# Kernel optimization log

Measured on AMD Instinct MI355X. Metric: run time of the kernel, lower is better.

Reference implementation:

```python
import jax, jax.numpy as jnp
import numpy as np

B, S, N, C, D = 1, 6, 10000, 128, 4
HEADS, PTS = 4, 8
HF, WF = 28, 50
M = HF * WF


def setup_inputs() -> dict:
    key0 = jax.random.key(0)
    ks = jax.random.split(key0, 14)
    sc = C ** -0.5
    d = {}
    d["query"] = jax.random.normal(ks[0], (B, N, C), jnp.float32)
    d["key"] = jax.random.normal(ks[1], (S, M, B, C), jnp.float32)
    d["value"] = jax.random.normal(ks[2], (S, M, B, C), jnp.float32)
    d["query_pos"] = jax.random.normal(ks[3], (B, N, C), jnp.float32) * 0.1
    d["reference_points_cam"] = jax.random.uniform(ks[4], (S, B, N, D, 2), jnp.float32, -0.2, 1.2)
    d["bev_mask"] = jax.random.randint(ks[5], (S, B, N, D), 0, 2).astype(bool)
    d["w_off"] = jax.random.normal(ks[6], (C, HEADS * PTS * 2), jnp.float32) * sc
    d["b_off"] = jax.random.normal(ks[7], (HEADS * PTS * 2,), jnp.float32) * 0.01
    d["w_attn"] = jax.random.normal(ks[8], (C, HEADS * PTS), jnp.float32) * sc
    d["b_attn"] = jax.random.normal(ks[9], (HEADS * PTS,), jnp.float32) * 0.01
    d["w_val"] = jax.random.normal(ks[10], (C, C), jnp.float32) * sc
    d["b_val"] = jax.random.normal(ks[11], (C,), jnp.float32) * 0.01
    d["w_out"] = jax.random.normal(ks[12], (C, C), jnp.float32) * sc
    d["b_out"] = jax.random.normal(ks[13], (C,), jnp.float32) * 0.01
    d["Hf"] = HF
    d["Wf"] = WF
    return d


def reference(query, key, value, query_pos, reference_points_cam, bev_mask,
              w_off, b_off, w_attn, b_attn, w_val, b_val, w_out, b_out, Hf, Wf):
    # SpatialCrossAttention with MSDeformAttn3D (BEVFormer semantics, eval mode: dropout=identity).
    # The torch data-dependent gather/rebatch/scatter is replaced by mathematically equivalent
    # masked computation: deformable attention is per-query independent, so running it for all
    # BEV queries per camera and mask-accumulating yields identical slots.
    B_, N_, C_ = query.shape
    S_ = key.shape[0]
    D_ = reference_points_cam.shape[3]
    H, P = HEADS, PTS
    dh = C_ // H
    Pd = P // D_
    q = query + query_pos  # (B,N,C)
    off = (q @ w_off + b_off).reshape(B_, N_, H, Pd, D_, 2)
    aw = jax.nn.softmax((q @ w_attn + b_attn).reshape(B_, N_, H, P), axis=-1)  # over levels*points (L=1)
    # value projection; per-camera feature maps laid out as (B,S,H,Hf*Wf,dh)
    v = jnp.transpose(value, (2, 0, 1, 3))  # (B,S,M,C)
    v = v @ w_val + b_val
    v = v.reshape(B_, S_, Hf * Wf, H, dh).transpose(0, 1, 3, 2, 4)  # (B,S,H,M,dh)
    ref = jnp.transpose(reference_points_cam, (1, 0, 2, 3, 4))  # (B,S,N,D,2)
    norm = jnp.array([Wf, Hf], jnp.float32)  # offset_normalizer = (W, H)
    loc = ref[:, :, :, None, None, :, :] + off[:, None] / norm  # (B,S,N,H,Pd,D,2)
    loc = loc.reshape(B_, S_, N_, H, P, 2)
    # bilinear sampling, zero padding, align_corners=False
    ix = loc[..., 0] * Wf - 0.5
    iy = loc[..., 1] * Hf - 0.5
    x0 = jnp.floor(ix)
    y0 = jnp.floor(iy)

    def flat(a):  # (B,S,N,H,P) -> (B,S,H,N*P)
        return a.transpose(0, 1, 3, 2, 4).reshape(B_, S_, H, N_ * P)

    def gather(xi, yi):
        ok = (xi >= 0) & (xi < Wf) & (yi >= 0) & (yi < Hf)
        xi_c = jnp.clip(xi, 0, Wf - 1).astype(jnp.int32)
        yi_c = jnp.clip(yi, 0, Hf - 1).astype(jnp.int32)
        idx = flat(yi_c * Wf + xi_c)
        g = jnp.take_along_axis(v, idx[..., None], axis=3)  # (B,S,H,N*P,dh)
        return g * flat(ok.astype(v.dtype))[..., None]

    wx1 = ix - x0
    wy1 = iy - y0
    wx0 = 1.0 - wx1
    wy0 = 1.0 - wy1
    samp = (gather(x0, y0) * flat(wx0 * wy0)[..., None]
            + gather(x0 + 1, y0) * flat(wx1 * wy0)[..., None]
            + gather(x0, y0 + 1) * flat(wx0 * wy1)[..., None]
            + gather(x0 + 1, y0 + 1) * flat(wx1 * wy1)[..., None])  # (B,S,H,N*P,dh)
    samp = samp.reshape(B_, S_, H, N_, P, dh)
    out = jnp.einsum('bshnpd,bnhp->bsnhd', samp, aw).reshape(B_, S_, N_, C_)
    # masked scatter-accumulate back to BEV slots
    mask = jnp.transpose(jnp.any(bev_mask, axis=-1), (1, 0, 2))  # (B,S,N)
    slots = jnp.sum(out * mask[..., None].astype(out.dtype), axis=1)  # (B,N,C)
    count = jnp.maximum(mask.astype(out.dtype).sum(axis=1), 1.0)
    slots = slots / count[..., None]
    return slots @ w_out + b_out + query  # dropout is identity in eval
```

## Files before the change

kernel.cpp:

```cpp
#include <hip/hip_runtime.h>
#include <math.h>

#define S_ 6
#define N_ 10000
#define C_ 128
#define D_ 4
#define H_ 4
#define P_ 8
#define HF_ 28
#define WF_ 50
#define M_ (HF_ * WF_)
#define DH_ 32
#define SM_ (S_ * M_)
#define QB_ 8
#define ABYTES (S_ * H_ * M_ * 32)

#define NB_V ((SM_ + 31) / 32)
#define NB_O ((N_ + 31) / 32)

typedef float floatx2 __attribute__((ext_vector_type(2)));
typedef _Float16 half4v __attribute__((ext_vector_type(4)));

template <int NC, int MT, int MR, int MODE>
__device__ __forceinline__ void gemm_body(
    const float* __restrict__ A, const float* __restrict__ A2,
    const float* __restrict__ B0, const float* __restrict__ B1,
    const float* __restrict__ bias0, const float* __restrict__ bias1,
    float* __restrict__ outf, char* __restrict__ out8,
    int Mrows, int m0, int tid, int nthreads, float (*Alds)[132]) {
  constexpr int NTHR = (NC / 4) * (MT / MR);

  for (int i = tid; i < MT * 32; i += nthreads) {
    int r = i >> 5, k = (i & 31) * 4;
    int row = m0 + r;
    float4 v = make_float4(0.f, 0.f, 0.f, 0.f);
    if (row < Mrows) {
      v = *(const float4*)(A + (size_t)row * C_ + k);
      if (MODE == 1) {
        float4 v2 = *(const float4*)(A2 + (size_t)row * C_ + k);
        v.x += v2.x; v.y += v2.y; v.z += v2.z; v.w += v2.w;
      }
    }
    *(float4*)(&Alds[r][k]) = v;
  }
  __syncthreads();
  if (tid >= NTHR) return;

  int ci = tid % (NC / 4);
  int mi = tid / (NC / 4);
  int c0 = ci * 4, r0 = mi * MR;

  const float* bs;
  if (MODE == 1) bs = (c0 < 64) ? bias0 + c0 : bias1 + (c0 - 64);
  else bs = bias0 + c0;

  float acc[MR][4];
#pragma unroll
  for (int j = 0; j < MR; ++j)
#pragma unroll
    for (int cc = 0; cc < 4; ++cc) acc[j][cc] = bs[cc];

#pragma unroll 2
  for (int k4 = 0; k4 < C_; k4 += 4) {
    float bf[16];
#pragma unroll
    for (int kk = 0; kk < 4; ++kk) {
      int k = k4 + kk;
      float4 b4;
      if (MODE == 1)
        b4 = (c0 < 64) ? *(const float4*)(B0 + (size_t)k * 64 + c0)
                       : *(const float4*)(B1 + (size_t)k * 32 + (c0 - 64));
      else
        b4 = *(const float4*)(B0 + (size_t)k * NC + c0);
      bf[kk * 4 + 0] = b4.x; bf[kk * 4 + 1] = b4.y;
      bf[kk * 4 + 2] = b4.z; bf[kk * 4 + 3] = b4.w;
    }
    float af[MR * 4];
#pragma unroll
    for (int j = 0; j < MR; ++j) {
      float4 a4 = *(const float4*)(&Alds[r0 + j][k4]);
      af[j * 4 + 0] = a4.x; af[j * 4 + 1] = a4.y;
      af[j * 4 + 2] = a4.z; af[j * 4 + 3] = a4.w;
    }
#pragma unroll
    for (int j = 0; j < MR; ++j)
#pragma unroll
      for (int kk = 0; kk < 4; ++kk)
#pragma unroll
        for (int cc = 0; cc < 4; ++cc)
          acc[j][cc] = fmaf(af[j * 4 + kk], bf[kk * 4 + cc], acc[j][cc]);
  }

#pragma unroll
  for (int j = 0; j < MR; ++j) {
    int row = m0 + r0 + j;
    if (row >= Mrows) continue;
    if (MODE == 0) {
      int s = row / M_, mm = row % M_;
      int y = mm / WF_, x = mm % WF_;
      int h = c0 >> 5, d0 = c0 & 31;
      int w = __builtin_amdgcn_cvt_pk_fp8_f32(acc[j][0], acc[j][1], 0, false);
      w = __builtin_amdgcn_cvt_pk_fp8_f32(acc[j][2], acc[j][3], w, true);
      size_t hm = (size_t)s * H_ + h;
      *(int*)(out8 + (hm * M_ + mm) * 32 + d0) = w;
      if (x > 0) {
        int kp = (x - 1) >> 1, slot = 1 - (x & 1);
        *(int*)(out8 + ABYTES + ((hm * HF_ + y) * 25 + kp) * 64 +
                slot * 32 + d0) = w;
      }
    } else if (MODE == 1) {
      *(float4*)(outf + (size_t)row * 96 + c0) =
          make_float4(acc[j][0], acc[j][1], acc[j][2], acc[j][3]);
    }
  }
}

__global__ __launch_bounds__(256) void prep_kernel(
    const float* __restrict__ value, const float* __restrict__ w_val,
    const float* __restrict__ b_val, char* __restrict__ vh8,
    const float* __restrict__ query, const float* __restrict__ query_pos,
    const float* __restrict__ w_off, const float* __restrict__ b_off,
    const float* __restrict__ w_attn, const float* __restrict__ b_attn,
    float* __restrict__ OFFL) {
  __shared__ float Alds[32][132];
  int bid = blockIdx.x;
  if (bid < NB_V) {
    gemm_body<128, 32, 4, 0>(value, nullptr, w_val, nullptr, b_val, nullptr,
                             nullptr, vh8, SM_, bid * 32, threadIdx.x, 256,
                             Alds);
  } else {
    gemm_body<96, 32, 4, 1>(query, query_pos, w_off, w_attn, b_off, b_attn,
                            OFFL, nullptr, N_, (bid - NB_V) * 32, threadIdx.x,
                            256, Alds);
  }
}

__global__ __launch_bounds__(256) void attn2_kernel(
    const float* __restrict__ OFFL,
    const float* __restrict__ refpts,
    const int*   __restrict__ bev_mask,
    const char*  __restrict__ vh8,
    const float* __restrict__ query,
    const float* __restrict__ w_out,
    const float* __restrict__ b_out,
    float* __restrict__ out) {
  int n0 = blockIdx.x * QB_;
  int tid = threadIdx.x;

  __shared__ float off[QB_][64];
  __shared__ float logits[QB_][32];
  __shared__ float aw[QB_][32];
  __shared__ float refl[QB_][48];
  __shared__ int smask[QB_][6];
  __shared__ int2 sidx[QB_][194];
  __shared__ half4v swh[QB_][194];
  __shared__ float sl[QB_][132];

  for (int i = tid; i < QB_ * 96; i += 256) {
    int q = i / 96, c = i % 96;
    float v = OFFL[(size_t)(n0 + q) * 96 + c];
    if (c < 64) off[q][c] = v; else logits[q][c - 64] = v;
  }
  for (int i = tid; i < QB_ * 48; i += 256) {
    int q = i / 48, rem = i % 48;
    int s = rem >> 3, r8 = rem & 7;
    refl[q][rem] = refpts[((size_t)s * N_ + (n0 + q)) * 8 + r8];
  }
  if (tid < QB_ * 6) {
    int q = tid / 6, s = tid % 6;
    const int* bm = bev_mask + ((size_t)s * N_ + (n0 + q)) * D_;
    smask[q][s] = (bm[0] | bm[1] | bm[2] | bm[3]) ? 1 : 0;
  }
  __syncthreads();

  {
    int q = tid >> 5, j = tid & 31, h = j >> 3;
    float mx = -1e30f;
#pragma unroll
    for (int p = 0; p < P_; ++p) mx = fmaxf(mx, logits[q][h * P_ + p]);
    float sum = 0.f;
#pragma unroll
    for (int p = 0; p < P_; ++p) sum += expf(logits[q][h * P_ + p] - mx);
    aw[q][j] = expf(logits[q][j] - mx) / sum;
  }
  __syncthreads();

  for (int i = tid; i < QB_ * 192; i += 256) {
    int q = i / 192, j = i % 192;
    int s = j >> 5, w32 = j & 31, p = w32 >> 2, h = w32 & 3;
    int pd = p >> 2, dd = p & 3;
    float rx = refl[q][s * 8 + dd * 2 + 0];
    float ry = refl[q][s * 8 + dd * 2 + 1];
    float ox = off[q][h * 16 + pd * 8 + dd * 2 + 0];
    float oy = off[q][h * 16 + pd * 8 + dd * 2 + 1];
    float ix = rx * (float)WF_ + ox - 0.5f;
    float iy = ry * (float)HF_ + oy - 0.5f;
    float x0f = floorf(ix), y0f = floorf(iy);
    int x0 = (int)x0f, y0 = (int)y0f;
    float wx1 = ix - x0f, wy1 = iy - y0f;
    float wx0 = 1.f - wx1, wy0 = 1.f - wy1;
    float a = aw[q][h * P_ + p];
    bool vx0 = (x0 >= 0) && (x0 < WF_);
    bool vx1 = (x0 + 1 >= 0) && (x0 + 1 < WF_);
    bool vy0 = (y0 >= 0) && (y0 < HF_);
    bool vy1 = (y0 + 1 >= 0) && (y0 + 1 < HF_);
    int y0c = min(max(y0, 0), HF_ - 1);
    int y1c = min(max(y0 + 1, 0), HF_ - 1);
    int hm = s * H_ + h;
    int itop, ibot;
    if (x0 >= 0 && x0 <= WF_ - 2 && !(x0 & 1)) {
      itop = (hm * M_ + y0c * WF_ + x0) * 32;
      ibot = (hm * M_ + y1c * WF_ + x0) * 32;
    } else if (x0 >= 1 && x0 <= WF_ - 1 && (x0 & 1)) {
      int kp = (x0 - 1) >> 1;
      itop = ABYTES + ((hm * HF_ + y0c) * 25 + kp) * 64;
      ibot = ABYTES + ((hm * HF_ + y1c) * 25 + kp) * 64;
    } else if (x0 == -1) {
      itop = (hm * M_ + y0c * WF_) * 32 - 32;
      ibot = (hm * M_ + y1c * WF_) * 32 - 32;
    } else {
      itop = ibot = 0;
    }
    float w00 = (vx0 && vy0) ? wx0 * wy0 * a : 0.f;
    float w10 = (vx1 && vy0) ? wx1 * wy0 * a : 0.f;
    float w01 = (vx0 && vy1) ? wx0 * wy1 * a : 0.f;
    float w11 = (vx1 && vy1) ? wx1 * wy1 * a : 0.f;
    sidx[q][j] = make_int2(itop, ibot);
    half4v wv = {(_Float16)w00, (_Float16)w10, (_Float16)w01, (_Float16)w11};
    swh[q][j] = wv;
  }
  __syncthreads();

  {
    int q = tid >> 5, t = tid & 31, h = t >> 3, c8 = t & 7;
    bool hi = (c8 & 4) != 0;
    const char* vb = vh8 + c8 * 8;
    float av[8] = {0.f, 0.f, 0.f, 0.f, 0.f, 0.f, 0.f, 0.f};
    for (int s = 0; s < S_; ++s) {
      if (!smask[q][s]) continue;
#pragma unroll
      for (int p = 0; p < P_; ++p) {
        int j = s * 32 + p * 4 + h;
        int2 I = sidx[q][j];
        half4v W = swh[q][j];
        float wt = hi ? (float)W[1] : (float)W[0];
        float wb = hi ? (float)W[3] : (float)W[2];
        int2 ta = *(const int2*)(vb + I.x);
        int2 tb = *(const int2*)(vb + I.y);
        floatx2 t0 = __builtin_amdgcn_cvt_pk_f32_fp8(ta.x, false);
        floatx2 t1 = __builtin_amdgcn_cvt_pk_f32_fp8(ta.x, true);
        floatx2 t2 = __builtin_amdgcn_cvt_pk_f32_fp8(ta.y, false);
        floatx2 t3 = __builtin_amdgcn_cvt_pk_f32_fp8(ta.y, true);
        av[0] = fmaf(t0.x, wt, av[0]); av[1] = fmaf(t0.y, wt, av[1]);
        av[2] = fmaf(t1.x, wt, av[2]); av[3] = fmaf(t1.y, wt, av[3]);
        av[4] = fmaf(t2.x, wt, av[4]); av[5] = fmaf(t2.y, wt, av[5]);
        av[6] = fmaf(t3.x, wt, av[6]); av[7] = fmaf(t3.y, wt, av[7]);
        floatx2 b0 = __builtin_amdgcn_cvt_pk_f32_fp8(tb.x, false);
        floatx2 b1 = __builtin_amdgcn_cvt_pk_f32_fp8(tb.x, true);
        floatx2 b2 = __builtin_amdgcn_cvt_pk_f32_fp8(tb.y, false);
        floatx2 b3 = __builtin_amdgcn_cvt_pk_f32_fp8(tb.y, true);
        av[0] = fmaf(b0.x, wb, av[0]); av[1] = fmaf(b0.y, wb, av[1]);
        av[2] = fmaf(b1.x, wb, av[2]); av[3] = fmaf(b1.y, wb, av[3]);
        av[4] = fmaf(b2.x, wb, av[4]); av[5] = fmaf(b2.y, wb, av[5]);
        av[6] = fmaf(b3.x, wb, av[6]); av[7] = fmaf(b3.y, wb, av[7]);
      }
    }
#pragma unroll
    for (int k = 0; k < 8; ++k) av[k] += __shfl_xor(av[k], 4);

    if (!hi) {
      int cnt = smask[q][0] + smask[q][1] + smask[q][2] +
                smask[q][3] + smask[q][4] + smask[q][5];
      float inv = 1.f / (float)(cnt > 0 ? cnt : 1);
      float* dst = &sl[q][h * DH_ + (c8 & 3) * 8];
#pragma unroll
      for (int k = 0; k < 8; ++k) dst[k] = av[k] * inv;
    }
  }
  __syncthreads();

  {
    int q2 = tid >> 5, c0 = (tid & 31) * 4;
    int n = n0 + q2;
    float4 qv = *(const float4*)(query + (size_t)n * C_ + c0);
    float4 bv = *(const float4*)(b_out + c0);
    float r0 = bv.x + qv.x, r1 = bv.y + qv.y;
    float r2 = bv.z + qv.z, r3 = bv.w + qv.w;
#pragma unroll 4
    for (int k = 0; k < C_; ++k) {
      float a = sl[q2][k];
      float4 w4 = *(const float4*)(w_out + (size_t)k * C_ + c0);
      r0 = fmaf(a, w4.x, r0); r1 = fmaf(a, w4.y, r1);
      r2 = fmaf(a, w4.z, r2); r3 = fmaf(a, w4.w, r3);
    }
    *(float4*)(out + (size_t)n * C_ + c0) = make_float4(r0, r1, r2, r3);
  }
}

extern "C" void kernel_launch(void* const* d_in, const int* in_sizes, int n_in,
                              void* d_out, int out_size, void* d_ws, size_t ws_size,
                              hipStream_t stream) {
  const float* query     = (const float*)d_in[0];
  const float* value     = (const float*)d_in[2];
  const float* query_pos = (const float*)d_in[3];
  const float* refpts    = (const float*)d_in[4];
  const int*   bev_mask  = (const int*)d_in[5];
  const float* w_off     = (const float*)d_in[6];
  const float* b_off     = (const float*)d_in[7];
  const float* w_attn    = (const float*)d_in[8];
  const float* b_attn    = (const float*)d_in[9];
  const float* w_val     = (const float*)d_in[10];
  const float* b_val     = (const float*)d_in[11];
  const float* w_out     = (const float*)d_in[12];
  const float* b_out     = (const float*)d_in[13];

  char* ws = (char*)d_ws;
  char* vh8   = ws + 64;
  float* OFFL = (float*)(ws + 64 + 2 * (size_t)ABYTES + 64);

  prep_kernel<<<NB_V + NB_O, 256, 0, stream>>>(
      value, w_val, b_val, vh8, query, query_pos, w_off, b_off, w_attn, b_attn,
      OFFL);
  attn2_kernel<<<N_ / QB_, 256, 0, stream>>>(OFFL, refpts, bev_mask, vh8,
                                             query, w_out, b_out,
                                             (float*)d_out);
}
```

Measured before the change: 158.7 us.

## Fold camera mask into sample weights and flatten gather loop branch-free

The per-camera mask is folded into the attention weights, so the gather loop runs a fixed 48 iterations with no per-camera branch. Masked cameras now get zero weight but are still gathered. Shared memory is packed into one aliased buffer, with the slot array reusing the offset/logit region behind an extra barrier. Weights are stored as per-lane half2 pairs so each lane reads only its own weights without a select. The aim is to cut divergence and shared-memory footprint for higher occupancy, but it spends extra gathers on roughly half of the camera slots, which are masked.

```diff
diff --git a/kernel.cpp b/kernel.cpp
--- a/kernel.cpp
+++ b/kernel.cpp
@@ -19,7 +19,7 @@
 #define NB_O ((N_ + 31) / 32)
 
 typedef float floatx2 __attribute__((ext_vector_type(2)));
-typedef _Float16 half4v __attribute__((ext_vector_type(4)));
+typedef _Float16 half2v __attribute__((ext_vector_type(2)));
 
 template <int NC, int MT, int MR, int MODE>
 __device__ __forceinline__ void gemm_body(
@@ -139,7 +139,7 @@
     const float* __restrict__ OFFL,
     const float* __restrict__ refpts,
     const int*   __restrict__ bev_mask,
-    const char*  __restrict__ vh8,
+    const char*  __restrict__ wsbase,
     const float* __restrict__ query,
     const float* __restrict__ w_out,
     const float* __restrict__ b_out,
@@ -147,29 +147,30 @@
   int n0 = blockIdx.x * QB_;
   int tid = threadIdx.x;
 
-  __shared__ float off[QB_][64];
-  __shared__ float logits[QB_][32];
-  __shared__ float aw[QB_][32];
-  __shared__ float refl[QB_][48];
-  __shared__ int smask[QB_][6];
-  __shared__ int2 sidx[QB_][194];
-  __shared__ half4v swh[QB_][194];
-  __shared__ float sl[QB_][132];
+  __shared__ char smem[30656];
+  int2*   sidx  = (int2*)smem;
+  half2v* swh   = (half2v*)(smem + 12416);
+  float*  offp  = (float*)(smem + 24832);
+  float*  logtp = (float*)(smem + 24832 + 2048);
+  float*  awp   = (float*)(smem + 24832 + 3072);
+  float*  reflp = (float*)(smem + 24832 + 4096);
+  float*  slp   = (float*)(smem + 24832);
+  int*    smaskp= (int*)(smem + 30464);
 
   for (int i = tid; i < QB_ * 96; i += 256) {
     int q = i / 96, c = i % 96;
     float v = OFFL[(size_t)(n0 + q) * 96 + c];
-    if (c < 64) off[q][c] = v; else logits[q][c - 64] = v;
+    if (c < 64) offp[q * 64 + c] = v; else logtp[q * 32 + c - 64] = v;
   }
   for (int i = tid; i < QB_ * 48; i += 256) {
     int q = i / 48, rem = i % 48;
     int s = rem >> 3, r8 = rem & 7;
-    refl[q][rem] = refpts[((size_t)s * N_ + (n0 + q)) * 8 + r8];
+    reflp[q * 48 + rem] = refpts[((size_t)s * N_ + (n0 + q)) * 8 + r8];
   }
   if (tid < QB_ * 6) {
     int q = tid / 6, s = tid % 6;
     const int* bm = bev_mask + ((size_t)s * N_ + (n0 + q)) * D_;
-    smask[q][s] = (bm[0] | bm[1] | bm[2] | bm[3]) ? 1 : 0;
+    smaskp[tid] = (bm[0] | bm[1] | bm[2] | bm[3]) ? 1 : 0;
   }
   __syncthreads();
 
@@ -177,11 +178,11 @@
     int q = tid >> 5, j = tid & 31, h = j >> 3;
     float mx = -1e30f;
 #pragma unroll
-    for (int p = 0; p < P_; ++p) mx = fmaxf(mx, logits[q][h * P_ + p]);
+    for (int p = 0; p < P_; ++p) mx = fmaxf(mx, logtp[q * 32 + h * P_ + p]);
     float sum = 0.f;
 #pragma unroll
-    for (int p = 0; p < P_; ++p) sum += expf(logits[q][h * P_ + p] - mx);
-    aw[q][j] = expf(logits[q][j] - mx) / sum;
+    for (int p = 0; p < P_; ++p) sum += expf(logtp[q * 32 + h * P_ + p] - mx);
+    awp[q * 32 + j] = expf(logtp[q * 32 + j] - mx) / sum;
   }
   __syncthreads();
 
@@ -189,17 +190,17 @@
     int q = i / 192, j = i % 192;
     int s = j >> 5, w32 = j & 31, p = w32 >> 2, h = w32 & 3;
     int pd = p >> 2, dd = p & 3;
-    float rx = refl[q][s * 8 + dd * 2 + 0];
-    float ry = refl[q][s * 8 + dd * 2 + 1];
-    float ox = off[q][h * 16 + pd * 8 + dd * 2 + 0];
-    float oy = off[q][h * 16 + pd * 8 + dd * 2 + 1];
+    float rx = reflp[q * 48 + s * 8 + dd * 2 + 0];
+    float ry = reflp[q * 48 + s * 8 + dd * 2 + 1];
+    float ox = offp[q * 64 + h * 16 + pd * 8 + dd * 2 + 0];
+    float oy = offp[q * 64 + h * 16 + pd * 8 + dd * 2 + 1];
     float ix = rx * (float)WF_ + ox - 0.5f;
     float iy = ry * (float)HF_ + oy - 0.5f;
     float x0f = floorf(ix), y0f = floorf(iy);
     int x0 = (int)x0f, y0 = (int)y0f;
     float wx1 = ix - x0f, wy1 = iy - y0f;
     float wx0 = 1.f - wx1, wy0 = 1.f - wy1;
-    float a = aw[q][h * P_ + p];
+    float a = awp[q * 32 + h * P_ + p] * (float)smaskp[q * 6 + s];
     bool vx0 = (x0 >= 0) && (x0 < WF_);
     bool vx1 = (x0 + 1 >= 0) && (x0 + 1 < WF_);
     bool vy0 = (y0 >= 0) && (y0 < HF_);
@@ -225,54 +226,55 @@
     float w10 = (vx1 && vy0) ? wx1 * wy0 * a : 0.f;
     float w01 = (vx0 && vy1) ? wx0 * wy1 * a : 0.f;
     float w11 = (vx1 && vy1) ? wx1 * wy1 * a : 0.f;
-    sidx[q][j] = make_int2(itop, ibot);
-    half4v wv = {(_Float16)w00, (_Float16)w10, (_Float16)w01, (_Float16)w11};
-    swh[q][j] = wv;
+    sidx[q * 194 + j] = make_int2(itop + 64, ibot + 64);
+    half2v lo = {(_Float16)w00, (_Float16)w01};
+    half2v hi = {(_Float16)w10, (_Float16)w11};
+    swh[(q * 194 + j) * 2 + 0] = lo;
+    swh[(q * 194 + j) * 2 + 1] = hi;
   }
   __syncthreads();
 
   {
     int q = tid >> 5, t = tid & 31, h = t >> 3, c8 = t & 7;
-    bool hi = (c8 & 4) != 0;
-    const char* vb = vh8 + c8 * 8;
+    int hisel = (c8 >> 2) & 1;
+    int lanebyte = c8 * 8;
+    const int2* sx = sidx + q * 194;
+    const half2v* swq = swh + (q * 194) * 2 + hisel;
     float av[8] = {0.f, 0.f, 0.f, 0.f, 0.f, 0.f, 0.f, 0.f};
-    for (int s = 0; s < S_; ++s) {
-      if (!smask[q][s]) continue;
-#pragma unroll
-      for (int p = 0; p < P_; ++p) {
-        int j = s * 32 + p * 4 + h;
-        int2 I = sidx[q][j];
-        half4v W = swh[q][j];
-        float wt = hi ? (float)W[1] : (float)W[0];
-        float wb = hi ? (float)W[3] : (float)W[2];
-        int2 ta = *(const int2*)(vb + I.x);
-        int2 tb = *(const int2*)(vb + I.y);
-        floatx2 t0 = __builtin_amdgcn_cvt_pk_f32_fp8(ta.x, false);
-        floatx2 t1 = __builtin_amdgcn_cvt_pk_f32_fp8(ta.x, true);
-        floatx2 t2 = __builtin_amdgcn_cvt_pk_f32_fp8(ta.y, false);
-        floatx2 t3 = __builtin_amdgcn_cvt_pk_f32_fp8(ta.y, true);
-        av[0] = fmaf(t0.x, wt, av[0]); av[1] = fmaf(t0.y, wt, av[1]);
-        av[2] = fmaf(t1.x, wt, av[2]); av[3] = fmaf(t1.y, wt, av[3]);
-        av[4] = fmaf(t2.x, wt, av[4]); av[5] = fmaf(t2.y, wt, av[5]);
-        av[6] = fmaf(t3.x, wt, av[6]); av[7] = fmaf(t3.y, wt, av[7]);
-        floatx2 b0 = __builtin_amdgcn_cvt_pk_f32_fp8(tb.x, false);
-        floatx2 b1 = __builtin_amdgcn_cvt_pk_f32_fp8(tb.x, true);
-        floatx2 b2 = __builtin_amdgcn_cvt_pk_f32_fp8(tb.y, false);
-        floatx2 b3 = __builtin_amdgcn_cvt_pk_f32_fp8(tb.y, true);
-        av[0] = fmaf(b0.x, wb, av[0]); av[1] = fmaf(b0.y, wb, av[1]);
-        av[2] = fmaf(b1.x, wb, av[2]); av[3] = fmaf(b1.y, wb, av[3]);
-        av[4] = fmaf(b2.x, wb, av[4]); av[5] = fmaf(b2.y, wb, av[5]);
-        av[6] = fmaf(b3.x, wb, av[6]); av[7] = fmaf(b3.y, wb, av[7]);
-      }
+#pragma unroll 4
+    for (int u = 0; u < 48; ++u) {
+      int j = (u >> 3) * 32 + (u & 7) * 4 + h;
+      int2 I = sx[j];
+      half2v w2 = swq[j * 2];
+      float wt = (float)w2[0], wb = (float)w2[1];
+      int2 ta = *(const int2*)(wsbase + (I.x + lanebyte));
+      int2 tb = *(const int2*)(wsbase + (I.y + lanebyte));
+      floatx2 t0 = __builtin_amdgcn_cvt_pk_f32_fp8(ta.x, false);
+      floatx2 t1 = __builtin_amdgcn_cvt_pk_f32_fp8(ta.x, true);
+      floatx2 t2 = __builtin_amdgcn_cvt_pk_f32_fp8(ta.y, false);
+      floatx2 t3 = __builtin_amdgcn_cvt_pk_f32_fp8(ta.y, true);
+      av[0] = fmaf(t0.x, wt, av[0]); av[1] = fmaf(t0.y, wt, av[1]);
+      av[2] = fmaf(t1.x, wt, av[2]); av[3] = fmaf(t1.y, wt, av[3]);
+      av[4] = fmaf(t2.x, wt, av[4]); av[5] = fmaf(t2.y, wt, av[5]);
+      av[6] = fmaf(t3.x, wt, av[6]); av[7] = fmaf(t3.y, wt, av[7]);
+      floatx2 b0 = __builtin_amdgcn_cvt_pk_f32_fp8(tb.x, false);
+      floatx2 b1 = __builtin_amdgcn_cvt_pk_f32_fp8(tb.x, true);
+      floatx2 b2 = __builtin_amdgcn_cvt_pk_f32_fp8(tb.y, false);
+      floatx2 b3 = __builtin_amdgcn_cvt_pk_f32_fp8(tb.y, true);
+      av[0] = fmaf(b0.x, wb, av[0]); av[1] = fmaf(b0.y, wb, av[1]);
+      av[2] = fmaf(b1.x, wb, av[2]); av[3] = fmaf(b1.y, wb, av[3]);
+      av[4] = fmaf(b2.x, wb, av[4]); av[5] = fmaf(b2.y, wb, av[5]);
+      av[6] = fmaf(b3.x, wb, av[6]); av[7] = fmaf(b3.y, wb, av[7]);
     }
 #pragma unroll
     for (int k = 0; k < 8; ++k) av[k] += __shfl_xor(av[k], 4);
 
-    if (!hi) {
-      int cnt = smask[q][0] + smask[q][1] + smask[q][2] +
-                smask[q][3] + smask[q][4] + smask[q][5];
-      float inv = 1.f / (float)(cnt > 0 ? cnt : 1);
-      float* dst = &sl[q][h * DH_ + (c8 & 3) * 8];
+    int cnt = smaskp[q * 6 + 0] + smaskp[q * 6 + 1] + smaskp[q * 6 + 2] +
+              smaskp[q * 6 + 3] + smaskp[q * 6 + 4] + smaskp[q * 6 + 5];
+    float inv = 1.f / (float)(cnt > 0 ? cnt : 1);
+    __syncthreads();
+    if (!hisel) {
+      float* dst = &slp[q * 132 + h * DH_ + (c8 & 3) * 8];
 #pragma unroll
       for (int k = 0; k < 8; ++k) dst[k] = av[k] * inv;
     }
@@ -288,7 +290,7 @@
     float r2 = bv.z + qv.z, r3 = bv.w + qv.w;
 #pragma unroll 4
     for (int k = 0; k < C_; ++k) {
-      float a = sl[q2][k];
+      float a = slp[q2 * 132 + k];
       float4 w4 = *(const float4*)(w_out + (size_t)k * C_ + c0);
       r0 = fmaf(a, w4.x, r0); r1 = fmaf(a, w4.y, r1);
       r2 = fmaf(a, w4.z, r2); r3 = fmaf(a, w4.w, r3);
@@ -321,7 +323,7 @@
   prep_kernel<<<NB_V + NB_O, 256, 0, stream>>>(
       value, w_val, b_val, vh8, query, query_pos, w_off, b_off, w_attn, b_attn,
       OFFL);
-  attn2_kernel<<<N_ / QB_, 256, 0, stream>>>(OFFL, refpts, bev_mask, vh8,
+  attn2_kernel<<<N_ / QB_, 256, 0, stream>>>(OFFL, refpts, bev_mask, ws,
                                              query, w_out, b_out,
                                              (float*)d_out);
 }
```

Measured after the change: 156.0 us. About the same (-1.7%).
